# Kernel optimization log

Measured on AMD Instinct MI355X. Metric: run time of the kernel, lower is better.

## Reference

```python
import jax, jax.numpy as jnp
import numpy as np

N = 4096
IN_F = 256
OUT_F = 128
H = 2
ALPHA = 0.2  # leaky relu slope
NEG_INF = -9e15  # matches -9000000000000000.0 in the torch code


def setup_inputs() -> dict:
    key = jax.random.key(0)
    k_x, k_adj, k_w, k_a = jax.random.split(key, 4)
    x = jax.random.normal(k_x, (N, IN_F), dtype=jnp.float32)
    adj = (jax.random.uniform(k_adj, (N, N)) < 0.005).astype(jnp.float32)
    # xavier_uniform with gain=1.414 as in the torch module
    gain = 1.414
    bound_w = gain * np.sqrt(6.0 / (IN_F + OUT_F))
    W = jax.random.uniform(k_w, (H, IN_F, OUT_F), minval=-bound_w, maxval=bound_w, dtype=jnp.float32)
    bound_a = gain * np.sqrt(6.0 / (2 * OUT_F + 1))
    a = jax.random.uniform(k_a, (H, 2 * OUT_F, 1), minval=-bound_a, maxval=bound_a, dtype=jnp.float32)
    return {"x": x, "adj": adj, "W": W, "a": a}


def reference(x, adj, W, a):
    # Dense multi-head GAT layer (eval mode: dropout is identity).
    n = x.shape[0]
    h, _, f_out = W.shape
    adj = adj + jnp.eye(n, dtype=adj.dtype)  # add self loops
    xt = jnp.einsum('nf,hfo->hno', x, W)  # [H, N, F_out]
    # The repeat_interleave/repeat + concat + matmul(a) in the original is
    # exactly the additive decomposition: score[h,i,j] = xt[h,i]@a1[h] + xt[h,j]@a2[h]
    a1 = a[:, :f_out, 0]   # [H, F_out] (applied to target/query node i)
    a2 = a[:, f_out:, 0]   # [H, F_out] (applied to source node j)
    e1 = jnp.einsum('hno,ho->hn', xt, a1)  # [H, N]
    e2 = jnp.einsum('hno,ho->hn', xt, a2)  # [H, N]
    scores = jax.nn.leaky_relu(e1[:, :, None] + e2[:, None, :], negative_slope=ALPHA)  # [H,N,N]
    scores = jnp.where(adj > 0, scores, jnp.asarray(NEG_INF, scores.dtype))
    attn = jax.nn.softmax(scores, axis=-1)
    h_prime = jnp.einsum('hij,hjo->hio', attn, xt)  # [H, N, F_out]
    # concat=True branch: torch .view(N, H*F_out) on contiguous [H,N,F] -> same as reshape
    return jax.nn.elu(h_prime.reshape(n, h * f_out))
```

## Files before the change

### kernel.cpp

```cpp
#include <hip/hip_runtime.h>
#include <math.h>

#define IN_F 256
#define OUT_F 128
#define NHEAD 2
#define ALPHA 0.2f
#define NN 4096
#define NCAP 256

typedef __attribute__((ext_vector_type(8))) short short8;
typedef __attribute__((ext_vector_type(4))) float f32x4;
typedef const __attribute__((address_space(1))) void* gas_ptr;
typedef __attribute__((address_space(3))) void* las_ptr;

__device__ __forceinline__ void async_copy16(const void* g, void* l) {
  __builtin_amdgcn_global_load_lds((gas_ptr)g, (las_ptr)l, 16, 0, 0);
}

__device__ __forceinline__ ushort f2bf(float f) {
  unsigned u = __float_as_uint(f);
  u += 0x7fffu + ((u >> 16) & 1u);
  return (ushort)(u >> 16);
}

__device__ __forceinline__ float lrelu(float t) { return t > 0.f ? t : ALPHA * t; }

__global__ __launch_bounds__(256) void prep_w(
    const float* __restrict__ W, ushort* __restrict__ Wt) {
  int p = blockIdx.x * 256 + threadIdx.x;
  int h = p >> 13;
  int rem = p & 8191;
  int c = rem >> 7;
  int o = rem & 127;
  const float* wsrc = W + h * (IN_F * OUT_F) + (4 * c) * OUT_F + o;
  ushort4 ov;
  ov.x = f2bf(wsrc[0 * OUT_F]);
  ov.y = f2bf(wsrc[1 * OUT_F]);
  ov.z = f2bf(wsrc[2 * OUT_F]);
  ov.w = f2bf(wsrc[3 * OUT_F]);
  *(ushort4*)(Wt + ((size_t)h * OUT_F + o) * IN_F + 4 * c) = ov;
}

__global__ __launch_bounds__(256) void gemm_mfma(
    const float* __restrict__ x, const ushort* __restrict__ Wt,
    const float* __restrict__ a,
    float* __restrict__ xt, float* __restrict__ e1, float* __restrict__ e2) {
  __shared__ ushort sA[32 * 64];
  __shared__ ushort sB[128 * 64];
  __shared__ float sa[2 * OUT_F];
  __shared__ float se1[32], se2[32];

  const int h = blockIdx.y;
  const int rowBase = blockIdx.x * 32;
  const int tid = threadIdx.x;
  const int wave = tid >> 6, lane = tid & 63;
  const int wr = wave & 1, wc = wave >> 1;
  const int q = lane >> 4, l16 = lane & 15;
  const int ar = tid >> 3;
  const int ak = (tid & 7) * 8;

  const float* xrow = x + (size_t)(rowBase + ar) * IN_F + ak;
  float4 ax[8];
#pragma unroll
  for (int c = 0; c < 4; ++c) {
    ax[2 * c]     = *(const float4*)(xrow + 64 * c);
    ax[2 * c + 1] = *(const float4*)(xrow + 64 * c + 4);
  }

  sa[tid] = a[h * (2 * OUT_F) + tid];

  f32x4 acc[4];
#pragma unroll
  for (int i = 0; i < 4; ++i) acc[i] = (f32x4)(0.0f);

  const char* wbase = (const char*)(Wt + (size_t)h * (OUT_F * IN_F));

#pragma unroll
  for (int c = 0; c < 4; ++c) {
    const int k0 = c * 64;
#pragma unroll
    for (int it = 0; it < 4; ++it) {
      int g = it * 256 + tid;
      int r = g >> 3, c8 = g & 7;
      async_copy16(wbase + r * 512 + k0 * 2 + c8 * 16,
                   (char*)sB + (size_t)(it * 256 + wave * 64) * 16);
    }
    {
      float4 va = ax[2 * c], vb = ax[2 * c + 1];
      union { short8 s8; ushort u[8]; } pk;
      pk.u[0] = f2bf(va.x); pk.u[1] = f2bf(va.y);
      pk.u[2] = f2bf(va.z); pk.u[3] = f2bf(va.w);
      pk.u[4] = f2bf(vb.x); pk.u[5] = f2bf(vb.y);
      pk.u[6] = f2bf(vb.z); pk.u[7] = f2bf(vb.w);
      *(short8*)(sA + ar * 64 + ak) = pk.s8;
    }
    __syncthreads();

#pragma unroll
    for (int ks = 0; ks < 64; ks += 32) {
      short8 af = *(const short8*)(sA + (wr * 16 + l16) * 64 + ks + q * 8);
#pragma unroll
      for (int ct = 0; ct < 4; ++ct) {
        int col = wc * 64 + ct * 16 + l16;
        short8 bf = *(const short8*)(sB + col * 64 + ks + q * 8);
        acc[ct] = __builtin_amdgcn_mfma_f32_16x16x32_bf16(af, bf, acc[ct], 0, 0, 0);
      }
    }
    __syncthreads();
  }

#pragma unroll
  for (int ct = 0; ct < 4; ++ct) {
    int col = wc * 64 + ct * 16 + l16;
#pragma unroll
    for (int reg = 0; reg < 4; ++reg) {
      int row = rowBase + wr * 16 + q * 4 + reg;
      xt[((size_t)h * NN + row) * OUT_F + col] = acc[ct][reg];
    }
  }

  float pe1[4], pe2[4];
#pragma unroll
  for (int reg = 0; reg < 4; ++reg) { pe1[reg] = 0.f; pe2[reg] = 0.f; }
#pragma unroll
  for (int ct = 0; ct < 4; ++ct) {
    int col = wc * 64 + ct * 16 + l16;
    float a1v = sa[col], a2v = sa[OUT_F + col];
#pragma unroll
    for (int reg = 0; reg < 4; ++reg) {
      pe1[reg] = fmaf(acc[ct][reg], a1v, pe1[reg]);
      pe2[reg] = fmaf(acc[ct][reg], a2v, pe2[reg]);
    }
  }
#pragma unroll
  for (int off = 1; off < 16; off <<= 1) {
#pragma unroll
    for (int reg = 0; reg < 4; ++reg) {
      pe1[reg] += __shfl_xor(pe1[reg], off, 64);
      pe2[reg] += __shfl_xor(pe2[reg], off, 64);
    }
  }
  if (wc == 0 && l16 == 0) {
#pragma unroll
    for (int reg = 0; reg < 4; ++reg) {
      int r = wr * 16 + q * 4 + reg;
      se1[r] = pe1[reg];
      se2[r] = pe2[reg];
    }
  }
  __syncthreads();
  if (wc == 1 && l16 == 0) {
#pragma unroll
    for (int reg = 0; reg < 4; ++reg) {
      int r = wr * 16 + q * 4 + reg;
      se1[r] += pe1[reg];
      se2[r] += pe2[reg];
    }
  }
  __syncthreads();
  if (tid < 32) {
    e1[(size_t)h * NN + rowBase + tid] = se1[tid];
    e2[(size_t)h * NN + rowBase + tid] = se2[tid];
  }
}

__global__ __launch_bounds__(256) void gat_aggregate(
    const float* __restrict__ adj, const float* __restrict__ xt,
    const float* __restrict__ e1, const float* __restrict__ e2,
    float* __restrict__ out) {
  __shared__ int s_nbr[NCAP];
  __shared__ float s_sc0[NCAP];
  __shared__ float s_sc1[NCAP];
  __shared__ int s_cnt;
  __shared__ float s_red[4][2];

  const int i = blockIdx.x;
  const int tid = threadIdx.x;
  const int wave = tid >> 6, lane = tid & 63;
  if (tid == 0) s_cnt = 0;
  __syncthreads();

  const float4* arow4 = (const float4*)(adj + (size_t)i * NN);
  float4 v[4];
#pragma unroll
  for (int it = 0; it < 4; ++it) v[it] = arow4[tid + it * 256];

#pragma unroll
  for (int it = 0; it < 4; ++it) {
    int j = (tid + it * 256) * 4;
    float vals[4] = {v[it].x, v[it].y, v[it].z, v[it].w};
#pragma unroll
    for (int s = 0; s < 4; ++s) {
      if (vals[s] > 0.f || j + s == i) {
        int p = atomicAdd(&s_cnt, 1);
        if (p < NCAP) s_nbr[p] = j + s;
      }
    }
  }
  __syncthreads();
  const int m = s_cnt < NCAP ? s_cnt : NCAP;

  const float e10 = e1[i];
  const float e11 = e1[NN + i];
  if (tid < m) {
    int j = s_nbr[tid];
    s_sc0[tid] = lrelu(e10 + e2[j]);
    s_sc1[tid] = lrelu(e11 + e2[NN + j]);
  }
  __syncthreads();

  float t0 = (tid < m) ? s_sc0[tid] : -3.0e38f;
  float t1 = (tid < m) ? s_sc1[tid] : -3.0e38f;
#pragma unroll
  for (int off = 32; off > 0; off >>= 1) {
    t0 = fmaxf(t0, __shfl_xor(t0, off, 64));
    t1 = fmaxf(t1, __shfl_xor(t1, off, 64));
  }
  if (lane == 0) { s_red[wave][0] = t0; s_red[wave][1] = t1; }
  __syncthreads();
  const float mx0 = fmaxf(fmaxf(s_red[0][0], s_red[1][0]), fmaxf(s_red[2][0], s_red[3][0]));
  const float mx1 = fmaxf(fmaxf(s_red[0][1], s_red[1][1]), fmaxf(s_red[2][1], s_red[3][1]));
  __syncthreads();

  float g0 = 0.f, g1 = 0.f;
  if (tid < m) {
    g0 = __expf(s_sc0[tid] - mx0); s_sc0[tid] = g0;
    g1 = __expf(s_sc1[tid] - mx1); s_sc1[tid] = g1;
  }
#pragma unroll
  for (int off = 32; off > 0; off >>= 1) {
    g0 += __shfl_xor(g0, off, 64);
    g1 += __shfl_xor(g1, off, 64);
  }
  if (lane == 0) { s_red[wave][0] = g0; s_red[wave][1] = g1; }
  __syncthreads();
  const float l0 = (s_red[0][0] + s_red[1][0]) + (s_red[2][0] + s_red[3][0]);
  const float l1 = (s_red[0][1] + s_red[1][1]) + (s_red[2][1] + s_red[3][1]);

  const int h = tid >> 7;
  const int o = tid & 127;
  const float* pp = h ? s_sc1 : s_sc0;
  const float linv = 1.0f / (h ? l1 : l0);
  const float* xth = xt + (size_t)h * NN * OUT_F + o;

  float acc = 0.f;
  int k = 0;
  for (; k + 4 <= m; k += 4) {
    int j0 = s_nbr[k], j1 = s_nbr[k + 1], j2 = s_nbr[k + 2], j3 = s_nbr[k + 3];
    float q0 = pp[k], q1 = pp[k + 1], q2 = pp[k + 2], q3 = pp[k + 3];
    float w0 = xth[(size_t)j0 * OUT_F], w1 = xth[(size_t)j1 * OUT_F];
    float w2 = xth[(size_t)j2 * OUT_F], w3 = xth[(size_t)j3 * OUT_F];
    acc = fmaf(q0, w0, acc); acc = fmaf(q1, w1, acc);
    acc = fmaf(q2, w2, acc); acc = fmaf(q3, w3, acc);
  }
  for (; k < m; ++k) acc = fmaf(pp[k], xth[(size_t)s_nbr[k] * OUT_F], acc);

  acc *= linv;
  float r = acc > 0.f ? acc : (__expf(acc) - 1.0f);
  out[((size_t)h * NN + i) * OUT_F + o] = r;
}

extern "C" void kernel_launch(void* const* d_in, const int* in_sizes, int n_in,
                              void* d_out, int out_size, void* d_ws, size_t ws_size,
                              hipStream_t stream) {
  const float* x   = (const float*)d_in[0];
  const float* adj = (const float*)d_in[1];
  const float* W   = (const float*)d_in[2];
  const float* a   = (const float*)d_in[3];
  float* out = (float*)d_out;

  float* xt = (float*)d_ws;
  float* e1 = xt + (size_t)NHEAD * NN * OUT_F;
  float* e2 = e1 + (size_t)NHEAD * NN;
  ushort* Wt = (ushort*)(e2 + (size_t)NHEAD * NN);

  prep_w<<<64, 256, 0, stream>>>(W, Wt);
  gemm_mfma<<<dim3(NN / 32, NHEAD), 256, 0, stream>>>(x, Wt, a, xt, e1, e2);
  gat_aggregate<<<NN, 256, 0, stream>>>(adj, xt, e1, e2, out);
}
```

Baseline: 115.4 us.

## Process one node per wave with ballot compaction and float4 gathers

The aggregation kernel now assigns one target row to each wavefront instead of one row per 256-thread block. Neighbour compaction uses ballot and popcount instead of shared-memory atomics, and the softmax reductions stay within the wave, so no block barriers are needed. The gather loop loads float4 chunks of xt per lane. The neighbour cap drops from 256 to 128, which is enough for this input's ~20 neighbours per row but would silently truncate denser rows.

```diff
diff --git a/kernel.cpp b/kernel.cpp
--- a/kernel.cpp
+++ b/kernel.cpp
@@ -6,7 +6,7 @@
 #define NHEAD 2
 #define ALPHA 0.2f
 #define NN 4096
-#define NCAP 256
+#define NCAP 128
 
 typedef __attribute__((ext_vector_type(8))) short short8;
 typedef __attribute__((ext_vector_type(4))) float f32x4;
@@ -168,96 +168,114 @@
     const float* __restrict__ adj, const float* __restrict__ xt,
     const float* __restrict__ e1, const float* __restrict__ e2,
     float* __restrict__ out) {
-  __shared__ int s_nbr[NCAP];
-  __shared__ float s_sc0[NCAP];
-  __shared__ float s_sc1[NCAP];
-  __shared__ int s_cnt;
-  __shared__ float s_red[4][2];
-
-  const int i = blockIdx.x;
-  const int tid = threadIdx.x;
-  const int wave = tid >> 6, lane = tid & 63;
-  if (tid == 0) s_cnt = 0;
-  __syncthreads();
-
-  const float4* arow4 = (const float4*)(adj + (size_t)i * NN);
-  float4 v[4];
-#pragma unroll
-  for (int it = 0; it < 4; ++it) v[it] = arow4[tid + it * 256];
-
-#pragma unroll
-  for (int it = 0; it < 4; ++it) {
-    int j = (tid + it * 256) * 4;
-    float vals[4] = {v[it].x, v[it].y, v[it].z, v[it].w};
+  __shared__ int s_nbr[4][NCAP];
+  __shared__ float s_p0[4][NCAP];
+  __shared__ float s_p1[4][NCAP];
+
+  const int wave = threadIdx.x >> 6;
+  const int lane = threadIdx.x & 63;
+  const int i = blockIdx.x * 4 + wave;
+
+  const float4* row4 = (const float4*)(adj + (size_t)i * NN);
+  float4 v[16];
+#pragma unroll
+  for (int c = 0; c < 16; ++c) v[c] = row4[lane + c * 64];
+
+  const unsigned long long lt = (1ull << lane) - 1ull;
+  int cnt = 0;
+#pragma unroll
+  for (int c = 0; c < 16; ++c) {
+    float vals[4] = {v[c].x, v[c].y, v[c].z, v[c].w};
 #pragma unroll
     for (int s = 0; s < 4; ++s) {
-      if (vals[s] > 0.f || j + s == i) {
-        int p = atomicAdd(&s_cnt, 1);
-        if (p < NCAP) s_nbr[p] = j + s;
+      int j = (c * 64 + lane) * 4 + s;
+      bool hit = (vals[s] > 0.f) || (j == i);
+      unsigned long long mask = __ballot(hit);
+      if (hit) {
+        int pos = cnt + (int)__popcll(mask & lt);
+        if (pos < NCAP) s_nbr[wave][pos] = j;
       }
-    }
-  }
-  __syncthreads();
-  const int m = s_cnt < NCAP ? s_cnt : NCAP;
+      cnt += (int)__popcll(mask);
+    }
+  }
+  const int m = cnt < NCAP ? cnt : NCAP;
 
   const float e10 = e1[i];
   const float e11 = e1[NN + i];
-  if (tid < m) {
-    int j = s_nbr[tid];
-    s_sc0[tid] = lrelu(e10 + e2[j]);
-    s_sc1[tid] = lrelu(e11 + e2[NN + j]);
-  }
-  __syncthreads();
-
-  float t0 = (tid < m) ? s_sc0[tid] : -3.0e38f;
-  float t1 = (tid < m) ? s_sc1[tid] : -3.0e38f;
+  float t0[2], t1[2];
+  float mx0 = -3.0e38f, mx1 = -3.0e38f;
+#pragma unroll
+  for (int r = 0; r < 2; ++r) {
+    int k = lane + r * 64;
+    if (k < m) {
+      int j = s_nbr[wave][k];
+      t0[r] = lrelu(e10 + e2[j]);
+      t1[r] = lrelu(e11 + e2[NN + j]);
+      mx0 = fmaxf(mx0, t0[r]);
+      mx1 = fmaxf(mx1, t1[r]);
+    } else {
+      t0[r] = -3.0e38f;
+      t1[r] = -3.0e38f;
+    }
+  }
 #pragma unroll
   for (int off = 32; off > 0; off >>= 1) {
-    t0 = fmaxf(t0, __shfl_xor(t0, off, 64));
-    t1 = fmaxf(t1, __shfl_xor(t1, off, 64));
-  }
-  if (lane == 0) { s_red[wave][0] = t0; s_red[wave][1] = t1; }
-  __syncthreads();
-  const float mx0 = fmaxf(fmaxf(s_red[0][0], s_red[1][0]), fmaxf(s_red[2][0], s_red[3][0]));
-  const float mx1 = fmaxf(fmaxf(s_red[0][1], s_red[1][1]), fmaxf(s_red[2][1], s_red[3][1]));
-  __syncthreads();
-
-  float g0 = 0.f, g1 = 0.f;
-  if (tid < m) {
-    g0 = __expf(s_sc0[tid] - mx0); s_sc0[tid] = g0;
-    g1 = __expf(s_sc1[tid] - mx1); s_sc1[tid] = g1;
+    mx0 = fmaxf(mx0, __shfl_xor(mx0, off, 64));
+    mx1 = fmaxf(mx1, __shfl_xor(mx1, off, 64));
+  }
+
+  float s0 = 0.f, s1 = 0.f;
+#pragma unroll
+  for (int r = 0; r < 2; ++r) {
+    int k = lane + r * 64;
+    if (k < m) {
+      float p0 = __expf(t0[r] - mx0);
+      float p1 = __expf(t1[r] - mx1);
+      s_p0[wave][k] = p0;
+      s_p1[wave][k] = p1;
+      s0 += p0;
+      s1 += p1;
+    }
   }
 #pragma unroll
   for (int off = 32; off > 0; off >>= 1) {
-    g0 += __shfl_xor(g0, off, 64);
-    g1 += __shfl_xor(g1, off, 64);
-  }
-  if (lane == 0) { s_red[wave][0] = g0; s_red[wave][1] = g1; }
-  __syncthreads();
-  const float l0 = (s_red[0][0] + s_red[1][0]) + (s_red[2][0] + s_red[3][0]);
-  const float l1 = (s_red[0][1] + s_red[1][1]) + (s_red[2][1] + s_red[3][1]);
-
-  const int h = tid >> 7;
-  const int o = tid & 127;
-  const float* pp = h ? s_sc1 : s_sc0;
-  const float linv = 1.0f / (h ? l1 : l0);
-  const float* xth = xt + (size_t)h * NN * OUT_F + o;
-
-  float acc = 0.f;
+    s0 += __shfl_xor(s0, off, 64);
+    s1 += __shfl_xor(s1, off, 64);
+  }
+
+  const int h = lane >> 5;
+  const int o4 = (lane & 31) * 4;
+  const float linv = 1.0f / (h ? s1 : s0);
+  const float* pw = h ? s_p1[wave] : s_p0[wave];
+  const int* nb = s_nbr[wave];
+  const float* xth = xt + (size_t)h * NN * OUT_F + o4;
+
+  f32x4 acc = (f32x4)(0.0f);
   int k = 0;
   for (; k + 4 <= m; k += 4) {
-    int j0 = s_nbr[k], j1 = s_nbr[k + 1], j2 = s_nbr[k + 2], j3 = s_nbr[k + 3];
-    float q0 = pp[k], q1 = pp[k + 1], q2 = pp[k + 2], q3 = pp[k + 3];
-    float w0 = xth[(size_t)j0 * OUT_F], w1 = xth[(size_t)j1 * OUT_F];
-    float w2 = xth[(size_t)j2 * OUT_F], w3 = xth[(size_t)j3 * OUT_F];
-    acc = fmaf(q0, w0, acc); acc = fmaf(q1, w1, acc);
-    acc = fmaf(q2, w2, acc); acc = fmaf(q3, w3, acc);
-  }
-  for (; k < m; ++k) acc = fmaf(pp[k], xth[(size_t)s_nbr[k] * OUT_F], acc);
-
-  acc *= linv;
-  float r = acc > 0.f ? acc : (__expf(acc) - 1.0f);
-  out[((size_t)h * NN + i) * OUT_F + o] = r;
+    int j0 = nb[k], j1 = nb[k + 1], j2 = nb[k + 2], j3 = nb[k + 3];
+    float w0 = pw[k], w1 = pw[k + 1], w2 = pw[k + 2], w3 = pw[k + 3];
+    f32x4 x0 = *(const f32x4*)(xth + (size_t)j0 * OUT_F);
+    f32x4 x1 = *(const f32x4*)(xth + (size_t)j1 * OUT_F);
+    f32x4 x2 = *(const f32x4*)(xth + (size_t)j2 * OUT_F);
+    f32x4 x3 = *(const f32x4*)(xth + (size_t)j3 * OUT_F);
+    acc += w0 * x0;
+    acc += w1 * x1;
+    acc += w2 * x2;
+    acc += w3 * x3;
+  }
+  for (; k < m; ++k) {
+    f32x4 xv = *(const f32x4*)(xth + (size_t)nb[k] * OUT_F);
+    acc += pw[k] * xv;
+  }
+
+  f32x4 r;
+#pragma unroll
+  for (int e = 0; e < 4; ++e) {
+    float av = acc[e] * linv;
+    r[e] = av > 0.f ? av : (__expf(av) - 1.0f);
+  }
+  *(f32x4*)(out + ((size_t)h * NN + i) * OUT_F + o4) = r;
 }
 
 extern "C" void kernel_launch(void* const* d_in, const int* in_sizes, int n_in,
@@ -276,5 +294,5 @@
 
   prep_w<<<64, 256, 0, stream>>>(W, Wt);
   gemm_mfma<<<dim3(NN / 32, NHEAD), 256, 0, stream>>>(x, Wt, a, xt, e1, e2);
-  gat_aggregate<<<NN, 256, 0, stream>>>(adj, xt, e1, e2, out);
-}
+  gat_aggregate<<<NN / 4, 256, 0, stream>>>(adj, xt, e1, e2, out);
+}
```

Result: faster. 112.5 us, median of 2 (-2.5%).
